# Kernel optimization log

Measured on AMD Instinct MI355X. Metric: run time of the kernel, lower is better.

## Reference

```python
import jax, jax.numpy as jnp
import numpy as np
from math import comb

N_SEG = 100000      # number of Bezier segments
BEZ_ORDER = 3       # cubic Bezier -> 4 control points per segment
D = 3               # point dimension
BATCH, NPTS = 8, 1000000


def setup_inputs() -> dict:
    key = jax.random.key(0)
    k1, k2, k3 = jax.random.split(key, 3)
    # strictly ascending knot vector: cumsum of positive dx, starting at 0
    dx = jax.random.uniform(k1, (N_SEG,), dtype=jnp.float32, minval=0.5, maxval=1.5)
    x_knots = jnp.concatenate([jnp.zeros((1,), jnp.float32), jnp.cumsum(dx)])
    x_end = x_knots[-1]
    # eval points spread beyond [0, x_end) so the modulo wrap is exercised
    x_eval = jax.random.uniform(k2, (BATCH, NPTS), dtype=jnp.float32) * (2.0 * x_end) - 0.5 * x_end
    control_points = jax.random.normal(k3, (N_SEG, BEZ_ORDER + 1, D), dtype=jnp.float32)
    return {"x_knots": x_knots, "control_points": control_points, "x_eval": x_eval}


def _bernstein_basis(s, n):
    # s: [N] in [0,1] -> basis [N, n+1]; powers via cumprod (differentiable at s=0/1)
    binom = jnp.asarray([comb(n, k) for k in range(n + 1)], dtype=s.dtype)
    t = s[:, None]
    ones = jnp.ones_like(t)
    t_pow = jnp.cumprod(jnp.concatenate([ones, jnp.broadcast_to(t, (t.shape[0], n))], axis=1), axis=1)         # t^k
    u = 1.0 - t
    u_pow = jnp.cumprod(jnp.concatenate([ones, jnp.broadcast_to(u, (u.shape[0], n))], axis=1), axis=1)         # u^k
    return binom * t_pow * u_pow[:, ::-1]  # C(n,k) t^k (1-t)^(n-k)


def reference(x_knots, control_points, x_eval):
    n = control_points.shape[1] - 1
    d = control_points.shape[2]
    xstart = x_knots[:-1]                      # [n_seg]
    dx = x_knots[1:] - x_knots[:-1]            # [n_seg]
    # x_true = x_eval % xend  (Python modulo semantics, matches torch %)
    x_true = jnp.mod(x_eval.reshape(-1), x_knots[-1])        # [N]
    # bucket search: segment index such that xstart[i] <= x_true < xstart[i+1]
    idx = jnp.clip(jnp.searchsorted(xstart, x_true, side='right') - 1, 0, xstart.shape[0] - 1)
    s = (x_true - xstart[idx]) / dx[idx]                     # local param in [0,1)
    basis = _bernstein_basis(s, n)                           # [N, n+1]
    P = control_points[idx]                                  # gather: [N, n+1, d]
    vals = jnp.einsum('nk,nkd->nd', basis, P)                # [N, d]
    return vals.reshape(x_eval.shape + (d,)), idx.reshape(x_eval.shape)
```

## Files before the change

kernel.cpp:

```cpp
#include <hip/hip_runtime.h>
#include <hip/hip_fp16.h>
#include <math.h>

#define N_SEG 100000
#define LUT_BITS 18
#define LUT_SIZE (1 << LUT_BITS)
#define DELTA 0.03
#define PPT 4

using f32x4  = __attribute__((ext_vector_type(4))) float;
using u32x4  = __attribute__((ext_vector_type(4))) unsigned int;

#define WS_NEED ((size_t)LUT_SIZE * 64)

__device__ __forceinline__ unsigned packh(float lo, float hi) {
    unsigned a = (unsigned)__half_as_ushort(__float2half(lo));
    unsigned b = (unsigned)__half_as_ushort(__float2half(hi));
    return a | (b << 16);
}
__device__ __forceinline__ float h2f(unsigned w, int hi) {
    return __half2float(__ushort_as_half((unsigned short)(hi ? (w >> 16) : (w & 0xFFFFu))));
}

__device__ __forceinline__ float mod_reduce(float x, float xe) {
    float r = x;
    r = (x >= xe) ? (x - xe) : r;
    r = (x < 0.0f) ? (x + xe) : r;
    return r;
}

__global__ void __launch_bounds__(256)
build_rec_kernel(const float* __restrict__ xk, const float* __restrict__ cp,
                 u32x4* __restrict__ rec) {
    int j = blockIdx.x * blockDim.x + threadIdx.x;
    if (j >= LUT_SIZE) return;
    double Wd = (double)xk[N_SEG] / (double)LUT_SIZE;
    double t = (double)j * Wd - DELTA;
    int lo = 0, hi = N_SEG;
    while (lo < hi) {
        int mid = (lo + hi) >> 1;
        if ((double)xk[mid] <= t) lo = mid + 1; else hi = mid;
    }
    int base = lo - 1;
    base = base < 0 ? 0 : (base > N_SEG - 1 ? N_SEG - 1 : base);

    int validb = (base + 1 <= N_SEG - 1) ? 1 : 0;
    int ia = base;
    int ib = validb ? base + 1 : base;

    float x0a = xk[base];
    float x1a = xk[base + 1];
    int i2 = base + 2 > N_SEG ? N_SEG : base + 2;
    float x1b = xk[i2];

    const f32x4* pa = reinterpret_cast<const f32x4*>(cp + (size_t)ia * 12);
    const f32x4* pb = reinterpret_cast<const f32x4*>(cp + (size_t)ib * 12);
    f32x4 a0 = pa[0], a1 = pa[1], a2 = pa[2];
    f32x4 b0 = pb[0], b1 = pb[1], b2 = pb[2];

    u32x4 w0 = { __float_as_uint(x0a), __float_as_uint(x1a), __float_as_uint(x1b),
                 (unsigned)base | ((unsigned)validb << 31) };
    u32x4 w1 = { packh(a0.x, a0.y), packh(a0.z, a0.w),
                 packh(a1.x, a1.y), packh(a1.z, a1.w) };
    u32x4 w2 = { packh(a2.x, a2.y), packh(a2.z, a2.w),
                 packh(b0.x, b0.y), packh(b0.z, b0.w) };
    u32x4 w3 = { packh(b1.x, b1.y), packh(b1.z, b1.w),
                 packh(b2.x, b2.y), packh(b2.z, b2.w) };
    u32x4* line = rec + 4 * (size_t)j;
    line[0] = w0; line[1] = w1; line[2] = w2; line[3] = w3;
}

__device__ __forceinline__ void decode_blend(u32x4 h, u32x4 w1, u32x4 w2, u32x4 w3,
                                             float r, float* v, float* idxf) {
    unsigned bw = h.w;
    int base = (int)(bw & 0x7FFFFFFFu);
    float x0a = __uint_as_float(h.x);
    float x1a = __uint_as_float(h.y);
    float x1b = __uint_as_float(h.z);
    int c = ((x1a <= r) && (bw >> 31)) ? 1 : 0;
    int idx = base + c;
    float x0 = c ? x1a : x0a;
    float x1 = c ? x1b : x1a;
    float s = (r - x0) / (x1 - x0);

    unsigned cw0 = c ? w2.z : w1.x;
    unsigned cw1 = c ? w2.w : w1.y;
    unsigned cw2 = c ? w3.x : w1.z;
    unsigned cw3 = c ? w3.y : w1.w;
    unsigned cw4 = c ? w3.z : w2.x;
    unsigned cw5 = c ? w3.w : w2.y;

    float u = 1.0f - s;
    float s2 = s * s, u2 = u * u;
    float b0 = u2 * u;
    float b1 = (3.0f * s) * u2;
    float b2 = (3.0f * s2) * u;
    float b3 = s2 * s;

    float c0 = h2f(cw0, 0), c1  = h2f(cw0, 1);
    float c2 = h2f(cw1, 0), c3  = h2f(cw1, 1);
    float c4 = h2f(cw2, 0), c5  = h2f(cw2, 1);
    float c6 = h2f(cw3, 0), c7  = h2f(cw3, 1);
    float c8 = h2f(cw4, 0), c9  = h2f(cw4, 1);
    float c10 = h2f(cw5, 0), c11 = h2f(cw5, 1);

    v[0] = b0 * c0 + b1 * c3 + b2 * c6 + b3 * c9;
    v[1] = b0 * c1 + b1 * c4 + b2 * c7 + b3 * c10;
    v[2] = b0 * c2 + b1 * c5 + b2 * c8 + b3 * c11;
    *idxf = (float)idx;
}

__global__ void __launch_bounds__(256)
eval_kernel(const float* __restrict__ xk,
            const float* __restrict__ xev,
            float* __restrict__ out_vals,
            float* __restrict__ out_idx,
            const unsigned char* __restrict__ rec,
            int npts) {
    __shared__ unsigned char stage[4 * PPT * 4 * 64 * 16];
    int t = blockIdx.x * blockDim.x + threadIdx.x;
    int lane = threadIdx.x & 63;
    int wave = threadIdx.x >> 6;
    long i0 = (long)t * PPT;

    float xe = xk[N_SEG];
    float invW = (float)LUT_SIZE / xe;

    if (i0 + PPT - 1 < (long)npts) {
        f32x4 x4 = __builtin_nontemporal_load(reinterpret_cast<const f32x4*>(xev) + t);
        float r[PPT] = {x4.x, x4.y, x4.z, x4.w};
        const unsigned char* pa[PPT];
        #pragma unroll
        for (int q = 0; q < PPT; ++q) {
            r[q] = mod_reduce(r[q], xe);
            int j = (int)(r[q] * invW);
            j = j < 0 ? 0 : (j > LUT_SIZE - 1 ? LUT_SIZE - 1 : j);
            pa[q] = rec + ((size_t)j << 6);
        }
        unsigned wbase = (unsigned)wave * (PPT * 4 * 1024);
        #pragma unroll
        for (int q = 0; q < PPT; ++q) {
            #pragma unroll
            for (int k = 0; k < 4; ++k) {
                __builtin_amdgcn_global_load_lds(
                    (const __attribute__((address_space(1))) void*)(pa[q] + 16 * k),
                    (__attribute__((address_space(3))) void*)(stage + wbase + (q * 4 + k) * 1024),
                    16, 0, 0);
            }
        }
        asm volatile("s_waitcnt vmcnt(0)" ::: "memory");
        __builtin_amdgcn_sched_barrier(0);

        float vals[PPT * 3];
        float idxf[PPT];
        #pragma unroll
        for (int q = 0; q < PPT; ++q) {
            const u32x4* pl = reinterpret_cast<const u32x4*>(stage + wbase + q * 4096 + lane * 16);
            u32x4 h  = pl[0];
            u32x4 w1 = pl[64];
            u32x4 w2 = pl[128];
            u32x4 w3 = pl[192];
            decode_blend(h, w1, w2, w3, r[q], &vals[q * 3], &idxf[q]);
        }
        f32x4* ov = reinterpret_cast<f32x4*>(out_vals + (size_t)t * 12);
        #pragma unroll
        for (int q = 0; q < 3; ++q) {
            f32x4 o = {vals[4 * q], vals[4 * q + 1], vals[4 * q + 2], vals[4 * q + 3]};
            ov[q] = o;
        }
        f32x4 oi = {idxf[0], idxf[1], idxf[2], idxf[3]};
        reinterpret_cast<f32x4*>(out_idx)[t] = oi;
    } else {
        for (long i = i0; i < (long)npts && i < i0 + PPT; ++i) {
            float r = mod_reduce(xev[i], xe);
            int j = (int)(r * invW);
            j = j < 0 ? 0 : (j > LUT_SIZE - 1 ? LUT_SIZE - 1 : j);
            const u32x4* line = reinterpret_cast<const u32x4*>(rec + ((size_t)j << 6));
            u32x4 h = line[0], w1 = line[1], w2 = line[2], w3 = line[3];
            float v[3], idxf;
            decode_blend(h, w1, w2, w3, r, v, &idxf);
            out_vals[(size_t)i * 3 + 0] = v[0];
            out_vals[(size_t)i * 3 + 1] = v[1];
            out_vals[(size_t)i * 3 + 2] = v[2];
            out_idx[i] = idxf;
        }
    }
}

__global__ void __launch_bounds__(256)
eval_kernel_bs(const float* __restrict__ xk,
               const float* __restrict__ cp,
               const float* __restrict__ xev,
               float* __restrict__ out_vals,
               float* __restrict__ out_idx,
               int npts) {
    int i = blockIdx.x * blockDim.x + threadIdx.x;
    if (i >= npts) return;
    float xe = xk[N_SEG];
    float r = mod_reduce(xev[i], xe);
    int lo = 0, hi = N_SEG;
    while (lo < hi) {
        int mid = (lo + hi) >> 1;
        if (xk[mid] <= r) lo = mid + 1; else hi = mid;
    }
    int idx = lo - 1;
    if (idx < 0) idx = 0;
    float x0 = xk[idx];
    float s = (r - x0) / (xk[idx + 1] - x0);
    float u = 1.0f - s;
    float s2 = s * s, u2 = u * u;
    float b0 = u2 * u, b1f = (3.0f * s) * u2, b2f = (3.0f * s2) * u, b3f = s2 * s;
    const f32x4* p = reinterpret_cast<const f32x4*>(cp + (size_t)idx * 12);
    f32x4 pA = p[0], pB = p[1], pC = p[2];
    out_vals[(size_t)i * 3 + 0] = b0 * pA.x + b1f * pA.w + b2f * pB.z + b3f * pC.y;
    out_vals[(size_t)i * 3 + 1] = b0 * pA.y + b1f * pB.x + b2f * pB.w + b3f * pC.z;
    out_vals[(size_t)i * 3 + 2] = b0 * pA.z + b1f * pB.y + b2f * pC.x + b3f * pC.w;
    out_idx[i] = (float)idx;
}

extern "C" void kernel_launch(void* const* d_in, const int* in_sizes, int n_in,
                              void* d_out, int out_size, void* d_ws, size_t ws_size,
                              hipStream_t stream) {
    const float* xk  = (const float*)d_in[0];
    const float* cp  = (const float*)d_in[1];
    const float* xev = (const float*)d_in[2];
    int npts = in_sizes[2];

    float* out_vals = (float*)d_out;
    float* out_idx  = out_vals + (size_t)npts * 3;

    if (ws_size >= WS_NEED) {
        u32x4* rec = (u32x4*)d_ws;
        build_rec_kernel<<<(LUT_SIZE + 255) / 256, 256, 0, stream>>>(xk, cp, rec);
        long nthreads = ((long)npts + PPT - 1) / PPT;
        int nblocks  = (int)((nthreads + 255) / 256);
        eval_kernel<<<nblocks, 256, 0, stream>>>(xk, xev, out_vals, out_idx,
                                                 (const unsigned char*)d_ws, npts);
    } else {
        int nblocks = (npts + 255) / 256;
        eval_kernel_bs<<<nblocks, 256, 0, stream>>>(xk, cp, xev, out_vals, out_idx, npts);
    }
}
```

Baseline: 160.0 us.

## Split 64-byte LUT records into a compact index LUT plus per-segment records

```diff
diff --git a/kernel.cpp b/kernel.cpp
--- a/kernel.cpp
+++ b/kernel.cpp
@@ -8,10 +8,12 @@
 #define DELTA 0.03
 #define PPT 4
 
-using f32x4  = __attribute__((ext_vector_type(4))) float;
-using u32x4  = __attribute__((ext_vector_type(4))) unsigned int;
-
-#define WS_NEED ((size_t)LUT_SIZE * 64)
+using f32x4 = __attribute__((ext_vector_type(4))) float;
+using u32x4 = __attribute__((ext_vector_type(4))) unsigned int;
+
+#define LUT_OFF 0
+#define REC_OFF (1 << 20)
+#define WS_NEED (REC_OFF + (size_t)(N_SEG + 1) * 32)
 
 __device__ __forceinline__ unsigned packh(float lo, float hi) {
     unsigned a = (unsigned)__half_as_ushort(__float2half(lo));
@@ -30,8 +32,7 @@
 }
 
 __global__ void __launch_bounds__(256)
-build_rec_kernel(const float* __restrict__ xk, const float* __restrict__ cp,
-                 u32x4* __restrict__ rec) {
+build_lut_kernel(const float* __restrict__ xk, unsigned* __restrict__ lut4) {
     int j = blockIdx.x * blockDim.x + threadIdx.x;
     if (j >= LUT_SIZE) return;
     double Wd = (double)xk[N_SEG] / (double)LUT_SIZE;
@@ -43,52 +44,49 @@
     }
     int base = lo - 1;
     base = base < 0 ? 0 : (base > N_SEG - 1 ? N_SEG - 1 : base);
-
-    int validb = (base + 1 <= N_SEG - 1) ? 1 : 0;
-    int ia = base;
-    int ib = validb ? base + 1 : base;
-
-    float x0a = xk[base];
-    float x1a = xk[base + 1];
-    int i2 = base + 2 > N_SEG ? N_SEG : base + 2;
-    float x1b = xk[i2];
-
-    const f32x4* pa = reinterpret_cast<const f32x4*>(cp + (size_t)ia * 12);
-    const f32x4* pb = reinterpret_cast<const f32x4*>(cp + (size_t)ib * 12);
-    f32x4 a0 = pa[0], a1 = pa[1], a2 = pa[2];
-    f32x4 b0 = pb[0], b1 = pb[1], b2 = pb[2];
-
-    u32x4 w0 = { __float_as_uint(x0a), __float_as_uint(x1a), __float_as_uint(x1b),
-                 (unsigned)base | ((unsigned)validb << 31) };
-    u32x4 w1 = { packh(a0.x, a0.y), packh(a0.z, a0.w),
-                 packh(a1.x, a1.y), packh(a1.z, a1.w) };
-    u32x4 w2 = { packh(a2.x, a2.y), packh(a2.z, a2.w),
-                 packh(b0.x, b0.y), packh(b0.z, b0.w) };
-    u32x4 w3 = { packh(b1.x, b1.y), packh(b1.z, b1.w),
-                 packh(b2.x, b2.y), packh(b2.z, b2.w) };
-    u32x4* line = rec + 4 * (size_t)j;
-    line[0] = w0; line[1] = w1; line[2] = w2; line[3] = w3;
-}
-
-__device__ __forceinline__ void decode_blend(u32x4 h, u32x4 w1, u32x4 w2, u32x4 w3,
-                                             float r, float* v, float* idxf) {
-    unsigned bw = h.w;
-    int base = (int)(bw & 0x7FFFFFFFu);
-    float x0a = __uint_as_float(h.x);
-    float x1a = __uint_as_float(h.y);
-    float x1b = __uint_as_float(h.z);
-    int c = ((x1a <= r) && (bw >> 31)) ? 1 : 0;
-    int idx = base + c;
+    lut4[j] = (unsigned)base;
+}
+
+__global__ void __launch_bounds__(256)
+build_rec_kernel(const float* __restrict__ xk, const float* __restrict__ cp,
+                 u32x4* __restrict__ rec) {
+    int i = blockIdx.x * blockDim.x + threadIdx.x;
+    if (i > N_SEG) return;
+    if (i == N_SEG) {
+        u32x4 w0 = { __float_as_uint(xk[N_SEG]), __float_as_uint(xk[N_SEG] + 1.0f), 0u, 0u };
+        u32x4 w1 = { 0u, 0u, 0u, 0u };
+        rec[2 * (size_t)i] = w0;
+        rec[2 * (size_t)i + 1] = w1;
+        return;
+    }
+    float x0 = xk[i];
+    float x1 = xk[i + 1];
+    const f32x4* p = reinterpret_cast<const f32x4*>(cp + (size_t)i * 12);
+    f32x4 a0 = p[0], a1 = p[1], a2 = p[2];
+    u32x4 w0 = { __float_as_uint(x0), __float_as_uint(x1),
+                 packh(a0.x, a0.y), packh(a0.z, a0.w) };
+    u32x4 w1 = { packh(a1.x, a1.y), packh(a1.z, a1.w),
+                 packh(a2.x, a2.y), packh(a2.z, a2.w) };
+    rec[2 * (size_t)i]     = w0;
+    rec[2 * (size_t)i + 1] = w1;
+}
+
+__device__ __forceinline__ void blend_from_words(
+        float r, int base, u32x4 A0, u32x4 A1, u32x4 B0, u32x4 B1,
+        float* v, float* idxf) {
+    float x0a = __uint_as_float(A0.x);
+    float x1a = __uint_as_float(A0.y);
+    int c = ((x1a <= r) && (base < N_SEG - 1)) ? 1 : 0;
     float x0 = c ? x1a : x0a;
-    float x1 = c ? x1b : x1a;
-    float s = (r - x0) / (x1 - x0);
-
-    unsigned cw0 = c ? w2.z : w1.x;
-    unsigned cw1 = c ? w2.w : w1.y;
-    unsigned cw2 = c ? w3.x : w1.z;
-    unsigned cw3 = c ? w3.y : w1.w;
-    unsigned cw4 = c ? w3.z : w2.x;
-    unsigned cw5 = c ? w3.w : w2.y;
+    float x1 = c ? __uint_as_float(B0.y) : x1a;
+    float s  = (r - x0) / (x1 - x0);
+
+    unsigned cw0 = c ? B0.z : A0.z;
+    unsigned cw1 = c ? B0.w : A0.w;
+    unsigned cw2 = c ? B1.x : A1.x;
+    unsigned cw3 = c ? B1.y : A1.y;
+    unsigned cw4 = c ? B1.z : A1.z;
+    unsigned cw5 = c ? B1.w : A1.w;
 
     float u = 1.0f - s;
     float s2 = s * s, u2 = u * u;
@@ -107,7 +105,7 @@
     v[0] = b0 * c0 + b1 * c3 + b2 * c6 + b3 * c9;
     v[1] = b0 * c1 + b1 * c4 + b2 * c7 + b3 * c10;
     v[2] = b0 * c2 + b1 * c5 + b2 * c8 + b3 * c11;
-    *idxf = (float)idx;
+    *idxf = (float)(base + c);
 }
 
 __global__ void __launch_bounds__(256)
@@ -115,12 +113,17 @@
             const float* __restrict__ xev,
             float* __restrict__ out_vals,
             float* __restrict__ out_idx,
-            const unsigned char* __restrict__ rec,
+            const unsigned char* __restrict__ ws,
             int npts) {
-    __shared__ unsigned char stage[4 * PPT * 4 * 64 * 16];
+    __shared__ u32x4 stage[4 * PPT * 4 * 64];
+    unsigned char* stg = reinterpret_cast<unsigned char*>(stage);
+    const unsigned* lut4 = reinterpret_cast<const unsigned*>(ws + LUT_OFF);
+    const unsigned char* rec = ws + REC_OFF;
+
     int t = blockIdx.x * blockDim.x + threadIdx.x;
     int lane = threadIdx.x & 63;
     int wave = threadIdx.x >> 6;
+    unsigned wbase = (unsigned)wave * (PPT * 4 * 1024);
     long i0 = (long)t * PPT;
 
     float xe = xk[N_SEG];
@@ -129,22 +132,35 @@
     if (i0 + PPT - 1 < (long)npts) {
         f32x4 x4 = __builtin_nontemporal_load(reinterpret_cast<const f32x4*>(xev) + t);
         float r[PPT] = {x4.x, x4.y, x4.z, x4.w};
-        const unsigned char* pa[PPT];
         #pragma unroll
         for (int q = 0; q < PPT; ++q) {
             r[q] = mod_reduce(r[q], xe);
             int j = (int)(r[q] * invW);
             j = j < 0 ? 0 : (j > LUT_SIZE - 1 ? LUT_SIZE - 1 : j);
-            pa[q] = rec + ((size_t)j << 6);
-        }
-        unsigned wbase = (unsigned)wave * (PPT * 4 * 1024);
-        #pragma unroll
-        for (int q = 0; q < PPT; ++q) {
+            __builtin_amdgcn_global_load_lds(
+                (const __attribute__((address_space(1))) void*)(lut4 + j),
+                (__attribute__((address_space(3))) void*)(stg + wbase + q * 256 + lane * 4),
+                4, 0, 0);
+        }
+        asm volatile("s_waitcnt vmcnt(0)" ::: "memory");
+        __builtin_amdgcn_sched_barrier(0);
+
+        int base[PPT];
+        #pragma unroll
+        for (int q = 0; q < PPT; ++q) {
+            base[q] = *reinterpret_cast<volatile int*>(stg + wbase + q * 256 + lane * 4);
+        }
+        asm volatile("s_waitcnt lgkmcnt(0)" ::: "memory");
+        __builtin_amdgcn_sched_barrier(0);
+
+        #pragma unroll
+        for (int q = 0; q < PPT; ++q) {
+            const unsigned char* w = rec + (size_t)base[q] * 32;
             #pragma unroll
             for (int k = 0; k < 4; ++k) {
                 __builtin_amdgcn_global_load_lds(
-                    (const __attribute__((address_space(1))) void*)(pa[q] + 16 * k),
-                    (__attribute__((address_space(3))) void*)(stage + wbase + (q * 4 + k) * 1024),
+                    (const __attribute__((address_space(1))) void*)(w + 16 * k),
+                    (__attribute__((address_space(3))) void*)(stg + wbase + (q * 4 + k) * 1024 + lane * 16),
                     16, 0, 0);
             }
         }
@@ -155,12 +171,12 @@
         float idxf[PPT];
         #pragma unroll
         for (int q = 0; q < PPT; ++q) {
-            const u32x4* pl = reinterpret_cast<const u32x4*>(stage + wbase + q * 4096 + lane * 16);
-            u32x4 h  = pl[0];
-            u32x4 w1 = pl[64];
-            u32x4 w2 = pl[128];
-            u32x4 w3 = pl[192];
-            decode_blend(h, w1, w2, w3, r[q], &vals[q * 3], &idxf[q]);
+            const u32x4* pl = reinterpret_cast<const u32x4*>(stg + wbase + q * 4096 + lane * 16);
+            u32x4 A0 = pl[0];
+            u32x4 A1 = pl[64];
+            u32x4 B0 = pl[128];
+            u32x4 B1 = pl[192];
+            blend_from_words(r[q], base[q], A0, A1, B0, B1, &vals[q * 3], &idxf[q]);
         }
         f32x4* ov = reinterpret_cast<f32x4*>(out_vals + (size_t)t * 12);
         #pragma unroll
@@ -175,14 +191,15 @@
             float r = mod_reduce(xev[i], xe);
             int j = (int)(r * invW);
             j = j < 0 ? 0 : (j > LUT_SIZE - 1 ? LUT_SIZE - 1 : j);
-            const u32x4* line = reinterpret_cast<const u32x4*>(rec + ((size_t)j << 6));
-            u32x4 h = line[0], w1 = line[1], w2 = line[2], w3 = line[3];
-            float v[3], idxf;
-            decode_blend(h, w1, w2, w3, r, v, &idxf);
+            int base = (int)lut4[j];
+            const u32x4* w = reinterpret_cast<const u32x4*>(rec + (size_t)base * 32);
+            u32x4 A0 = w[0], A1 = w[1], B0 = w[2], B1 = w[3];
+            float v[3], idxv;
+            blend_from_words(r, base, A0, A1, B0, B1, v, &idxv);
             out_vals[(size_t)i * 3 + 0] = v[0];
             out_vals[(size_t)i * 3 + 1] = v[1];
             out_vals[(size_t)i * 3 + 2] = v[2];
-            out_idx[i] = idxf;
+            out_idx[i] = idxv;
         }
     }
 }
@@ -230,12 +247,14 @@
     float* out_idx  = out_vals + (size_t)npts * 3;
 
     if (ws_size >= WS_NEED) {
-        u32x4* rec = (u32x4*)d_ws;
-        build_rec_kernel<<<(LUT_SIZE + 255) / 256, 256, 0, stream>>>(xk, cp, rec);
+        unsigned char* ws = (unsigned char*)d_ws;
+        unsigned* lut4 = (unsigned*)(ws + LUT_OFF);
+        u32x4*   rec   = (u32x4*)(ws + REC_OFF);
+        build_lut_kernel<<<(LUT_SIZE + 255) / 256, 256, 0, stream>>>(xk, lut4);
+        build_rec_kernel<<<(N_SEG + 1 + 255) / 256, 256, 0, stream>>>(xk, cp, rec);
         long nthreads = ((long)npts + PPT - 1) / PPT;
-        int nblocks  = (int)((nthreads + 255) / 256);
-        eval_kernel<<<nblocks, 256, 0, stream>>>(xk, xev, out_vals, out_idx,
-                                                 (const unsigned char*)d_ws, npts);
+        int nblocks = (int)((nthreads + 255) / 256);
+        eval_kernel<<<nblocks, 256, 0, stream>>>(xk, xev, out_vals, out_idx, ws, npts);
     } else {
         int nblocks = (npts + 255) / 256;
         eval_kernel_bs<<<nblocks, 256, 0, stream>>>(xk, cp, xev, out_vals, out_idx, npts);
```

After: 172.7 us. 1.08x slower.
